# Optimization experiments

Measured on AMD Instinct MI355X. Metric: run time of the kernel, lower is better.

Reference implementation:

```python
import jax, jax.numpy as jnp
import numpy as np

N_VERBS = 500
N_ROLES = 190
VOCAB = 2000
R = 6            # max_role_count
EMB = 512        # embed_hidden == lstm_hidden
MLP = 1024       # mlp_hidden
C = 512          # conv base size
H = W = 7
NP = H * W
NC = C + 2       # conv channels + 2 coord channels


def _lin(k, fan_in, fan_out):
    kw, kb = jax.random.split(k)
    s = 1.0 / np.sqrt(fan_in)
    return (jax.random.uniform(kw, (fan_in, fan_out), jnp.float32, -s, s),
            jax.random.uniform(kb, (fan_out,), jnp.float32, -s, s))


def setup_inputs() -> dict:
    key = jax.random.key(0)
    ks = jax.random.split(key, 16)
    inp = {}
    inp['conv_feat'] = jax.random.normal(ks[0], (2, C, H, W), jnp.float32)
    inp['verbs'] = jax.random.randint(ks[1], (2,), 0, N_VERBS, jnp.int32)
    inp['roles'] = jax.random.randint(ks[2], (2, R), 0, N_ROLES, jnp.int32)
    inp['verb_emb'] = jax.random.normal(ks[3], (N_VERBS, EMB), jnp.float32)
    inp['role_emb'] = jax.random.normal(ks[4], (N_ROLES + 1, EMB), jnp.float32)
    inp['vW1'], inp['vb1'] = _lin(ks[5], NP * C, MLP)
    inp['vW2'], inp['vb2'] = _lin(ks[6], MLP, MLP)
    inp['vW3'], inp['vb3'] = _lin(ks[7], MLP, N_VERBS)
    inp['gW1'], inp['gb1'] = _lin(ks[8], 2 * NC + EMB, MLP)
    inp['gW2'], inp['gb2'] = _lin(ks[9], MLP, MLP)
    inp['gW3'], inp['gb3'] = _lin(ks[10], MLP, 2 * MLP)
    inp['gW4'], inp['gb4'] = _lin(ks[11], 2 * MLP, 4 * MLP)
    inp['fW1'], inp['fb1'] = _lin(ks[12], 4 * MLP, 4 * MLP)
    inp['fW2'], inp['fb2'] = _lin(ks[13], 4 * MLP, 2 * MLP)
    inp['fW3'], inp['fb3'] = _lin(ks[14], 2 * MLP, VOCAB)
    return inp


def _coords():
    c = jnp.linspace(-4.0, 4.0, H)
    x = jnp.broadcast_to(c[None, :], (H, W))   # x varies along width
    y = jnp.broadcast_to(c[:, None], (H, W))   # y varies along height
    return jnp.stack([x, y]).reshape(2, NP).T  # [NP, 2]


def reference(conv_feat, verbs, roles, verb_emb, role_emb,
              vW1, vb1, vW2, vb2, vW3, vb3,
              gW1, gb1, gW2, gb2, gW3, gb3, gW4, gb4,
              fW1, fb1, fW2, fb2, fW3, fb3):
    relu = jax.nn.relu
    B = conv_feat.shape[0]

    # verb head
    flat = conv_feat.reshape(B, NP * C)
    v = relu(flat @ vW1 + vb1)
    v = relu(v @ vW2 + vb2)
    verb_pred = v @ vW3 + vb3                                  # [B, N_VERBS]

    # role-verb query
    rv = (verb_emb[verbs][:, None, :] * role_emb[roles]).reshape(B * R, EMB)

    # per-role conv features + coord channels -> [Bu, NP, NC]
    feat = jnp.broadcast_to(conv_feat[:, None], (B, R, C, H, W)).reshape(B * R, C, NP)
    feat = jnp.concatenate([feat.transpose(0, 2, 1),
                            jnp.broadcast_to(_coords()[None], (B * R, NP, 2))], axis=2)

    # first g layer: concat([o_j, o_i, qst]) @ gW1 == split matmuls + broadcast add
    Wa, Wb, Wc = gW1[:NC], gW1[NC:2 * NC], gW1[2 * NC:]
    A = feat @ Wa          # pairs with conv1 (index j)
    Bm = feat @ Wb         # pairs with conv2 (index i)
    Q = rv @ Wc
    h = relu(A[:, None, :, :] + Bm[:, :, None, :] + Q[:, None, None, :] + gb1)  # [Bu, NP, NP, MLP]
    h = relu(h @ gW2 + gb2)
    h = relu(h @ gW3 + gb3)
    h = relu(h @ gW4 + gb4)                                    # [Bu, NP, NP, 4*MLP]
    g = h.sum(axis=(1, 2))                                     # [Bu, 4*MLP]

    f = relu(g @ fW1 + fb1)
    f = relu(f @ fW2 + fb2)
    f = f @ fW3 + fb3                                          # [Bu, VOCAB]
    role_predict = f.reshape(B, R, VOCAB)
    return verb_pred, role_predict
```

## Files before the change

kernel.cpp:

```cpp
#include <hip/hip_runtime.h>
#include <cstdint>

typedef _Float16 f16;
typedef f16 f16x8 __attribute__((ext_vector_type(8)));
typedef f16 f16x4 __attribute__((ext_vector_type(4)));
typedef float f32x4 __attribute__((ext_vector_type(4)));

#define GROUP_ROWS 2560
#define VALID_ROWS 2401
#define TPG 10
#define NGROUP 12

template <bool B> struct BoolC { static constexpr bool value = B; };

__device__ __forceinline__ void gll16(const void* g, void* l) {
  __builtin_amdgcn_global_load_lds((const __attribute__((address_space(1))) void*)g,
                                   (__attribute__((address_space(3))) void*)l, 16, 0, 0);
}

__global__ void wtrans_all(const float* __restrict__ gW2, const float* __restrict__ gW3,
                           const float* __restrict__ gW4, f16* __restrict__ W2t,
                           f16* __restrict__ W3t, f16* __restrict__ W4t) {
  __shared__ float t[32][33];
  int blk = blockIdx.x;
  const float* W; f16* Wt; int K, N, local;
  if (blk < 1024)      { W = gW2; Wt = W2t; K = 1024; N = 1024; local = blk; }
  else if (blk < 3072) { W = gW3; Wt = W3t; K = 1024; N = 2048; local = blk - 1024; }
  else                 { W = gW4; Wt = W4t; K = 2048; N = 4096; local = blk - 3072; }
  int ntn = N >> 5;
  int k0 = (local / ntn) * 32, n0 = (local % ntn) * 32;
  int tx = threadIdx.x & 31, ty = threadIdx.x >> 5;
#pragma unroll
  for (int j = 0; j < 4; ++j)
    t[ty + j * 8][tx] = W[(size_t)(k0 + ty + j * 8) * N + n0 + tx];
  __syncthreads();
#pragma unroll
  for (int j = 0; j < 4; ++j)
    Wt[(size_t)(n0 + ty + j * 8) * K + k0 + tx] = (f16)t[tx][ty + j * 8];
}

__global__ void build_rv(const float* __restrict__ verb_emb, const float* __restrict__ role_emb,
                         const int* __restrict__ verbs, const int* __restrict__ roles,
                         float* __restrict__ rv) {
  int g = blockIdx.x;
  int b = g / 6;
  int v = verbs[b], ro = roles[g];
  for (int e = threadIdx.x; e < 512; e += 256)
    rv[g * 512 + e] = verb_emb[(size_t)v * 512 + e] * role_emb[(size_t)ro * 512 + e];
}

__global__ void build_AB(const float* __restrict__ conv, const float* __restrict__ gW1,
                         float* __restrict__ A, float* __restrict__ Bm) {
  int blk = blockIdx.x;
  int nq = blk & 3, bp = blk >> 2;
  int p = bp % 49, b = bp / 49;
  int n = nq * 256 + threadIdx.x;
  float accA = 0.f, accB = 0.f;
  for (int k = 0; k < 514; ++k) {
    float s;
    if (k < 512) s = conv[((size_t)b * 512 + k) * 49 + p];
    else {
      int c7 = (k == 512) ? (p % 7) : (p / 7);
      s = (float)(c7 - 3) * (4.0f / 3.0f);
    }
    accA = fmaf(s, gW1[(size_t)k * 1024 + n], accA);
    accB = fmaf(s, gW1[(size_t)(514 + k) * 1024 + n], accB);
  }
  size_t row = ((size_t)b * 49 + p) * 1024;
  A[row + n] = accA;
  Bm[row + n] = accB;
}

__global__ void build_h1(const float* __restrict__ A, const float* __restrict__ Bm,
                         const float* __restrict__ Q, const float* __restrict__ gb1,
                         f16* __restrict__ h1, int g0) {
  int rc = blockIdx.x;
  int gl = rc / GROUP_ROWS;
  int li = rc % GROUP_ROWS;
  int g = g0 + gl;
  int b = g / 6;
  int kk = threadIdx.x * 4;
  f16x4* dst = (f16x4*)(h1 + (size_t)rc * 1024 + kk);
  if (li >= VALID_ROWS) {
    f16x4 z = {(f16)0.f, (f16)0.f, (f16)0.f, (f16)0.f};
    *dst = z;
    return;
  }
  int i = li / 49, j = li % 49;
  const float4 a = *(const float4*)(A + ((size_t)b * 49 + j) * 1024 + kk);
  const float4 bb = *(const float4*)(Bm + ((size_t)b * 49 + i) * 1024 + kk);
  const float4 q = *(const float4*)(Q + (size_t)g * 1024 + kk);
  const float4 bi = *(const float4*)(gb1 + kk);
  float v0 = a.x + bb.x + q.x + bi.x;
  float v1 = a.y + bb.y + q.y + bi.y;
  float v2 = a.z + bb.z + q.z + bi.z;
  float v3 = a.w + bb.w + q.w + bi.w;
  f16x4 r;
  r.x = (f16)(v0 > 0.f ? v0 : 0.f);
  r.y = (f16)(v1 > 0.f ? v1 : 0.f);
  r.z = (f16)(v2 > 0.f ? v2 : 0.f);
  r.w = (f16)(v3 > 0.f ? v3 : 0.f);
  *dst = r;
}

#define WV4 asm volatile("s_waitcnt vmcnt(4)" ::: "memory")
#define WV0 asm volatile("s_waitcnt vmcnt(0)" ::: "memory")

#define LDSA(buf, mf, cc) (*(const f16x8*)(ldsc + (buf)*32768 + arow + (mf)*2048 + (cc)*16))
#define LDSB(buf, nf, cc) (*(const f16x8*)(ldsc + 65536 + (buf)*32768 + brow + (nf)*2048 + (cc)*16))

#define LOADB(BF, buf) { \
  BF[0][0] = LDSB(buf, 0, c0); BF[0][1] = LDSB(buf, 0, c1); \
  BF[1][0] = LDSB(buf, 1, c0); BF[1][1] = LDSB(buf, 1, c1); \
  BF[2][0] = LDSB(buf, 2, c0); BF[2][1] = LDSB(buf, 2, c1); \
  BF[3][0] = LDSB(buf, 3, c0); BF[3][1] = LDSB(buf, 3, c1); }

#define STAGE_A(t, h) { \
  const f16* _g = Aglo + (long)(h) * (128L * K) + (long)(t) * 64; \
  char* _l = ldsc + ((t)&1)*32768 + ((h)*128 + wave*16)*128; \
  gll16(_g, _l); gll16(_g + 8L*K, _l + 1024); }

#define STAGE_B(t, h) { \
  const f16* _g = Bglo + (long)(h) * (128L * K) + (long)(t) * 64; \
  char* _l = ldsc + 65536 + ((t)&1)*32768 + ((h)*128 + wave*16)*128; \
  gll16(_g, _l); gll16(_g + 8L*K, _l + 1024); }

#define PHASE(q, buf, BF, STG, WT, POST) { \
  f16x8 a00 = LDSA(buf, 2*(q), c0);   f16x8 a01 = LDSA(buf, 2*(q), c1); \
  f16x8 a10 = LDSA(buf, 2*(q)+1, c0); f16x8 a11 = LDSA(buf, 2*(q)+1, c1); \
  STG; \
  WT; \
  __builtin_amdgcn_s_barrier(); \
  __builtin_amdgcn_s_setprio(1); \
  _Pragma("unroll") \
  for (int nf = 0; nf < 4; ++nf) { \
    acc[2*(q)][nf]   = __builtin_amdgcn_mfma_f32_16x16x32_f16(a00, BF[nf][0], acc[2*(q)][nf], 0, 0, 0); \
    acc[2*(q)][nf]   = __builtin_amdgcn_mfma_f32_16x16x32_f16(a01, BF[nf][1], acc[2*(q)][nf], 0, 0, 0); \
    acc[2*(q)+1][nf] = __builtin_amdgcn_mfma_f32_16x16x32_f16(a10, BF[nf][0], acc[2*(q)+1][nf], 0, 0, 0); \
    acc[2*(q)+1][nf] = __builtin_amdgcn_mfma_f32_16x16x32_f16(a11, BF[nf][1], acc[2*(q)+1][nf], 0, 0, 0); \
  } \
  __builtin_amdgcn_s_setprio(0); \
  POST; \
  __builtin_amdgcn_s_barrier(); \
}

template <int FUSED>
__global__ __launch_bounds__(512, 2)
void gemm256(const f16* __restrict__ A, const f16* __restrict__ Bt,
             const float* __restrict__ bias, f16* __restrict__ C,
             float* __restrict__ P, int N, int K, int ntiles, int mtile_off) {
  __shared__ __align__(16) char ldsbuf[131072];
  char* ldsc = ldsbuf;
  const int tid = threadIdx.x;
  const int wave = tid >> 6, lane = tid & 63;
  const int wm = wave >> 2, wn = wave & 3;
  const int lr = lane & 15, lk = lane >> 4;
  const int c0 = lk ^ (lr & 7), c1 = c0 ^ 4;
  const int arow = (wm * 128 + lr) * 128;
  const int brow = (wn * 64 + lr) * 128;

  int nwg = gridDim.x, id = blockIdx.x;
  int qq = nwg >> 3, rr8 = nwg & 7;
  int xcd = id & 7, idx = id >> 3;
  int wg = (xcd < rr8 ? xcd * (qq + 1) : rr8 * (qq + 1) + (xcd - rr8) * qq) + idx;
  const int mtile = wg / ntiles, ntile = wg % ntiles;
  const long m0 = (long)mtile * 256, n0 = (long)ntile * 256;

  const int srow = lane >> 3;
  const int schunk = (lane & 7) ^ srow;
  const f16* Aglo = A + (m0 + wave * 16 + srow) * (long)K + schunk * 8;
  const f16* Bglo = Bt + (n0 + wave * 16 + srow) * (long)K + schunk * 8;

  f32x4 acc[8][4] = {};
  f16x8 bFa[4][2], bFb[4][2];

  const int NI = K >> 7;

  STAGE_B(0, 0); STAGE_B(0, 1);
  STAGE_A(0, 0); STAGE_A(0, 1);
  STAGE_B(1, 0); STAGE_B(1, 1);
  WV4;
  __builtin_amdgcn_s_barrier();
  LOADB(bFa, 0);

  auto run_iter = [&](int i, auto lastTag) {
    constexpr bool LAST = decltype(lastTag)::value;
    PHASE(0, 0, bFa, STAGE_A(2*i+1, 0), ;, ;);
    PHASE(1, 0, bFa, STAGE_A(2*i+1, 1), ;, ;);
    PHASE(2, 0, bFa, if constexpr (!LAST) STAGE_B(2*i+2, 0), ;, ;);
    PHASE(3, 0, bFa, if constexpr (!LAST) STAGE_B(2*i+2, 1),
                 if constexpr (LAST) { WV0; } else { WV4; },
                 LOADB(bFb, 1));
    PHASE(0, 1, bFb, if constexpr (!LAST) STAGE_A(2*i+2, 0), ;, ;);
    PHASE(1, 1, bFb, if constexpr (!LAST) STAGE_A(2*i+2, 1), ;, ;);
    PHASE(2, 1, bFb, if constexpr (!LAST) STAGE_B(2*i+3, 0), ;, ;);
    PHASE(3, 1, bFb, if constexpr (!LAST) STAGE_B(2*i+3, 1),
                 if constexpr (!LAST) { WV4; },
                 if constexpr (!LAST) LOADB(bFa, 0));
  };
#pragma unroll 1
  for (int i = 0; i < NI - 1; ++i) run_iter(i, BoolC<false>{});
  run_iter(NI - 1, BoolC<true>{});

  if (FUSED == 0) {
#pragma unroll
    for (int mf = 0; mf < 8; ++mf) {
      const long row = m0 + wm * 128 + mf * 16 + lk * 4;
#pragma unroll
      for (int nf = 0; nf < 4; ++nf) {
        const long col = n0 + wn * 64 + nf * 16 + lr;
        const float bv = bias[col];
#pragma unroll
        for (int r = 0; r < 4; ++r) {
          float v = acc[mf][nf][r] + bv;
          v = v > 0.f ? v : 0.f;
          C[(row + r) * N + col] = (f16)v;
        }
      }
    }
  } else {
    float* csum = (float*)ldsc;
    const int mrel = (mtile % TPG) * 256 + wm * 128;
#pragma unroll
    for (int nf = 0; nf < 4; ++nf) {
      const int col = (int)n0 + wn * 64 + nf * 16 + lr;
      const float bv = bias[col];
      float s = 0.f;
#pragma unroll
      for (int mf = 0; mf < 8; ++mf) {
        const int rb = mrel + mf * 16 + lk * 4;
#pragma unroll
        for (int r = 0; r < 4; ++r) {
          float v = acc[mf][nf][r] + bv;
          v = v > 0.f ? v : 0.f;
          if (rb + r < VALID_ROWS) s += v;
        }
      }
      s += __shfl_xor(s, 16);
      s += __shfl_xor(s, 32);
      if (lk == 0) csum[wm * 256 + wn * 64 + nf * 16 + lr] = s;
    }
    __syncthreads();
    for (int t = tid; t < 256; t += 512)
      P[(long)(mtile_off + mtile) * N + n0 + t] = csum[t] + csum[256 + t];
  }
}

__global__ void reduce_g(const float* __restrict__ P, float* __restrict__ g) {
  int idx = blockIdx.x * 256 + threadIdx.x;
  if (idx >= NGROUP * 4096) return;
  int gi = idx >> 12, n = idx & 4095;
  float s = 0.f;
#pragma unroll
  for (int t = 0; t < TPG; ++t) s += P[(size_t)(gi * TPG + t) * 4096 + n];
  g[idx] = s;
}

template <int M>
__global__ void skinny_part(const float* __restrict__ X, const float* __restrict__ W,
                            float* __restrict__ P, int K, int N, int kchunk) {
  int n = blockIdx.x * 256 + threadIdx.x;
  int k0 = blockIdx.y * kchunk;
  int k1 = k0 + kchunk;
  if (k1 > K) k1 = K;
  if (n >= N) return;
  float acc[M];
#pragma unroll
  for (int m = 0; m < M; ++m) acc[m] = 0.f;
  for (int k = k0; k < k1; ++k) {
    float w = W[(size_t)k * N + n];
#pragma unroll
    for (int m = 0; m < M; ++m) acc[m] = fmaf(X[(size_t)m * K + k], w, acc[m]);
  }
#pragma unroll
  for (int m = 0; m < M; ++m) P[((size_t)blockIdx.y * M + m) * N + n] = acc[m];
}

template <int RELU>
__global__ void skinny_fin(const float* __restrict__ P, const float* __restrict__ bias,
                           float* __restrict__ dst, int M, int N, int KC) {
  int idx = blockIdx.x * 256 + threadIdx.x;
  if (idx >= M * N) return;
  int m = idx / N, n = idx - m * N;
  float s = bias ? bias[n] : 0.f;
  for (int kc = 0; kc < KC; ++kc) s += P[((size_t)kc * M + m) * N + n];
  if (RELU) s = s > 0.f ? s : 0.f;
  dst[idx] = s;
}

static inline void skinny(const float* X, const float* W, const float* bias, float* dst,
                          float* sp, int Mrows, int K, int N, int relu, hipStream_t stream) {
  int KC = K >> 4;
  if (KC > 64) KC = 64;
  if (KC < 1) KC = 1;
  int kchunk = (K + KC - 1) / KC;
  dim3 g1((N + 255) / 256, KC);
  if (Mrows == 2)
    skinny_part<2><<<g1, 256, 0, stream>>>(X, W, sp, K, N, kchunk);
  else
    skinny_part<12><<<g1, 256, 0, stream>>>(X, W, sp, K, N, kchunk);
  int blocks = (Mrows * N + 255) / 256;
  if (relu)
    skinny_fin<1><<<blocks, 256, 0, stream>>>(sp, bias, dst, Mrows, N, KC);
  else
    skinny_fin<0><<<blocks, 256, 0, stream>>>(sp, bias, dst, Mrows, N, KC);
}

extern "C" void kernel_launch(void* const* d_in, const int* in_sizes, int n_in,
                              void* d_out, int out_size, void* d_ws, size_t ws_size,
                              hipStream_t stream) {
  const float* conv = (const float*)d_in[0];
  const int* verbs = (const int*)d_in[1];
  const int* roles = (const int*)d_in[2];
  const float* verb_emb = (const float*)d_in[3];
  const float* role_emb = (const float*)d_in[4];
  const float* vW1 = (const float*)d_in[5];
  const float* vb1 = (const float*)d_in[6];
  const float* vW2 = (const float*)d_in[7];
  const float* vb2 = (const float*)d_in[8];
  const float* vW3 = (const float*)d_in[9];
  const float* vb3 = (const float*)d_in[10];
  const float* gW1 = (const float*)d_in[11];
  const float* gb1 = (const float*)d_in[12];
  const float* gW2 = (const float*)d_in[13];
  const float* gb2 = (const float*)d_in[14];
  const float* gW3 = (const float*)d_in[15];
  const float* gb3 = (const float*)d_in[16];
  const float* gW4 = (const float*)d_in[17];
  const float* gb4 = (const float*)d_in[18];
  const float* fW1 = (const float*)d_in[19];
  const float* fb1 = (const float*)d_in[20];
  const float* fW2 = (const float*)d_in[21];
  const float* fb2 = (const float*)d_in[22];
  const float* fW3 = (const float*)d_in[23];
  const float* fb3 = (const float*)d_in[24];
  float* out = (float*)d_out;

  char* w = (char*)d_ws;
  auto alloc = [&](size_t bytes) {
    char* p = w;
    w += (bytes + 255) & ~(size_t)255;
    return p;
  };
  f16* W2t = (f16*)alloc((size_t)1024 * 1024 * 2);
  f16* W3t = (f16*)alloc((size_t)2048 * 1024 * 2);
  f16* W4t = (f16*)alloc((size_t)4096 * 2048 * 2);
  float* P4 = (float*)alloc((size_t)NGROUP * TPG * 4096 * 4);
  float* Abuf = (float*)alloc((size_t)2 * 49 * 1024 * 4);
  float* Bbuf = (float*)alloc((size_t)2 * 49 * 1024 * 4);
  float* Qbuf = (float*)alloc((size_t)12 * 1024 * 4);
  float* rvb = (float*)alloc((size_t)12 * 512 * 4);
  float* gbuf = (float*)alloc((size_t)12 * 4096 * 4);
  float* sp = (float*)alloc((size_t)64 * 12 * 4096 * 4);
  float* f1b = (float*)alloc((size_t)12 * 4096 * 4);
  float* f2b = (float*)alloc((size_t)12 * 2048 * 4);
  float* v1b = (float*)alloc((size_t)2 * 1024 * 4);
  float* v2b = (float*)alloc((size_t)2 * 1024 * 4);

  size_t used = (size_t)(w - (char*)d_ws);
  size_t remain = ws_size > used ? ws_size - used : 0;
  static const int opts[6] = {12, 6, 4, 3, 2, 1};
  int gpc = 1;
  for (int i = 0; i < 6; ++i) {
    size_t need = (size_t)opts[i] * GROUP_ROWS * 4096 * 2 + 4096;
    if (need <= remain) { gpc = opts[i]; break; }
  }
  f16* h1 = (f16*)alloc((size_t)gpc * GROUP_ROWS * 1024 * 2);
  f16* h2 = (f16*)alloc((size_t)gpc * GROUP_ROWS * 1024 * 2);
  f16* h3 = (f16*)alloc((size_t)gpc * GROUP_ROWS * 2048 * 2);
  int nchunks = NGROUP / gpc;

  wtrans_all<<<1024 + 2048 + 8192, 256, 0, stream>>>(gW2, gW3, gW4, W2t, W3t, W4t);

  build_rv<<<12, 256, 0, stream>>>(verb_emb, role_emb, verbs, roles, rvb);
  build_AB<<<98 * 4, 256, 0, stream>>>(conv, gW1, Abuf, Bbuf);
  skinny(rvb, gW1 + (size_t)1028 * 1024, nullptr, Qbuf, sp, 12, 512, 1024, 0, stream);

  skinny(conv, vW1, vb1, v1b, sp, 2, 25088, 1024, 1, stream);
  skinny(v1b, vW2, vb2, v2b, sp, 2, 1024, 1024, 1, stream);
  skinny(v2b, vW3, vb3, out, sp, 2, 1024, 500, 0, stream);

  for (int c = 0; c < nchunks; ++c) {
    int g0 = c * gpc;
    int Mc = gpc * GROUP_ROWS;
    int mt = Mc / 256;
    build_h1<<<Mc, 256, 0, stream>>>(Abuf, Bbuf, Qbuf, gb1, h1, g0);
    gemm256<0><<<4 * mt, 512, 0, stream>>>(h1, W2t, gb2, h2, nullptr, 1024, 1024, 4, 0);
    gemm256<0><<<8 * mt, 512, 0, stream>>>(h2, W3t, gb3, h3, nullptr, 2048, 1024, 8, 0);
    gemm256<1><<<16 * mt, 512, 0, stream>>>(h3, W4t, gb4, nullptr, P4, 4096, 2048, 16, g0 * TPG);
  }
  reduce_g<<<(NGROUP * 4096 + 255) / 256, 256, 0, stream>>>(P4, gbuf);

  skinny(gbuf, fW1, fb1, f1b, sp, 12, 4096, 4096, 1, stream);
  skinny(f1b, fW2, fb2, f2b, sp, 12, 4096, 2048, 1, stream);
  skinny(f2b, fW3, fb3, out + 1000, sp, 12, 2048, 2000, 0, stream);

  (void)in_sizes; (void)n_in; (void)out_size; (void)ws_size;
}
```

Baseline: 1.162 ms.

## Split-K AB build, stage GEMM epilogue through LDS, retune skinny split

Splits the A/B first-layer projection over eight K chunks with a separate reduction kernel, so more blocks run in parallel. Stages the non-fused GEMM epilogue through a swizzled LDS tile so stores become coalesced 16-byte row writes. Retunes the skinny split-K count to target about 1024 blocks and unrolls its inner loop. These add extra partial-sum buffer traffic and kernel launches. The split-K scratch must also fit in the shared sp buffer.

```diff
diff --git a/kernel.cpp b/kernel.cpp
--- a/kernel.cpp
+++ b/kernel.cpp
@@ -49,14 +49,17 @@
     rv[g * 512 + e] = verb_emb[(size_t)v * 512 + e] * role_emb[(size_t)ro * 512 + e];
 }
 
-__global__ void build_AB(const float* __restrict__ conv, const float* __restrict__ gW1,
-                         float* __restrict__ A, float* __restrict__ Bm) {
+__global__ void build_AB_part(const float* __restrict__ conv, const float* __restrict__ gW1,
+                              float* __restrict__ part) {
   int blk = blockIdx.x;
   int nq = blk & 3, bp = blk >> 2;
   int p = bp % 49, b = bp / 49;
   int n = nq * 256 + threadIdx.x;
+  int ky = blockIdx.y;
+  int k0 = ky * 66, k1 = k0 + 66;
+  if (k1 > 514) k1 = 514;
   float accA = 0.f, accB = 0.f;
-  for (int k = 0; k < 514; ++k) {
+  for (int k = k0; k < k1; ++k) {
     float s;
     if (k < 512) s = conv[((size_t)b * 512 + k) * 49 + p];
     else {
@@ -66,9 +69,21 @@
     accA = fmaf(s, gW1[(size_t)k * 1024 + n], accA);
     accB = fmaf(s, gW1[(size_t)(514 + k) * 1024 + n], accB);
   }
-  size_t row = ((size_t)b * 49 + p) * 1024;
-  A[row + n] = accA;
-  Bm[row + n] = accB;
+  size_t base = ((size_t)ky * 98 + bp) * 2048;
+  part[base + n] = accA;
+  part[base + 1024 + n] = accB;
+}
+
+__global__ void build_AB_fin(const float* __restrict__ part, float* __restrict__ A,
+                             float* __restrict__ Bm) {
+  int idx = blockIdx.x * 256 + threadIdx.x;
+  if (idx >= 98 * 2048) return;
+  int bp = idx >> 11, rem = idx & 2047;
+  float s = 0.f;
+#pragma unroll
+  for (int ky = 0; ky < 8; ++ky) s += part[((size_t)ky * 98 + bp) * 2048 + rem];
+  if (rem < 1024) A[(size_t)bp * 1024 + rem] = s;
+  else Bm[(size_t)bp * 1024 + (rem - 1024)] = s;
 }
 
 __global__ void build_h1(const float* __restrict__ A, const float* __restrict__ Bm,
@@ -203,20 +218,31 @@
   run_iter(NI - 1, BoolC<true>{});
 
   if (FUSED == 0) {
+    __syncthreads();
+    f16* lt = (f16*)ldsc;
 #pragma unroll
     for (int mf = 0; mf < 8; ++mf) {
-      const long row = m0 + wm * 128 + mf * 16 + lk * 4;
 #pragma unroll
       for (int nf = 0; nf < 4; ++nf) {
-        const long col = n0 + wn * 64 + nf * 16 + lr;
-        const float bv = bias[col];
+        const int col = wn * 64 + nf * 16 + lr;
+        const float bv = bias[n0 + col];
 #pragma unroll
         for (int r = 0; r < 4; ++r) {
+          const int row = wm * 128 + mf * 16 + lk * 4 + r;
           float v = acc[mf][nf][r] + bv;
           v = v > 0.f ? v : 0.f;
-          C[(row + r) * N + col] = (f16)v;
+          lt[row * 256 + (col ^ (((row >> 2) & 3) << 4))] = (f16)v;
         }
       }
+    }
+    __syncthreads();
+    const int r0 = tid >> 5, ch = tid & 31;
+#pragma unroll
+    for (int p = 0; p < 16; ++p) {
+      const int row = p * 16 + r0;
+      const int chs = ch ^ (((row >> 2) & 3) << 1);
+      f16x8 v = *(const f16x8*)(lt + row * 256 + chs * 8);
+      *(f16x8*)(C + (m0 + row) * N + n0 + ch * 8) = v;
     }
   } else {
     float* csum = (float*)ldsc;
@@ -267,6 +293,7 @@
   float acc[M];
 #pragma unroll
   for (int m = 0; m < M; ++m) acc[m] = 0.f;
+#pragma unroll 4
   for (int k = k0; k < k1; ++k) {
     float w = W[(size_t)k * N + n];
 #pragma unroll
@@ -290,11 +317,14 @@
 
 static inline void skinny(const float* X, const float* W, const float* bias, float* dst,
                           float* sp, int Mrows, int K, int N, int relu, hipStream_t stream) {
-  int KC = K >> 4;
-  if (KC > 64) KC = 64;
-  if (KC < 1) KC = 1;
+  int nx = (N + 255) / 256;
+  int KC = 1024 / nx;
+  if (KC > 256) KC = 256;
+  int kmax = K / 16;
+  if (kmax < 1) kmax = 1;
+  if (KC > kmax) KC = kmax;
   int kchunk = (K + KC - 1) / KC;
-  dim3 g1((N + 255) / 256, KC);
+  dim3 g1(nx, KC);
   if (Mrows == 2)
     skinny_part<2><<<g1, 256, 0, stream>>>(X, W, sp, K, N, kchunk);
   else
@@ -373,7 +403,8 @@
   wtrans_all<<<1024 + 2048 + 8192, 256, 0, stream>>>(gW2, gW3, gW4, W2t, W3t, W4t);
 
   build_rv<<<12, 256, 0, stream>>>(verb_emb, role_emb, verbs, roles, rvb);
-  build_AB<<<98 * 4, 256, 0, stream>>>(conv, gW1, Abuf, Bbuf);
+  build_AB_part<<<dim3(98 * 4, 8), 256, 0, stream>>>(conv, gW1, sp);
+  build_AB_fin<<<(98 * 2048 + 255) / 256, 256, 0, stream>>>(sp, Abuf, Bbuf);
   skinny(rvb, gW1 + (size_t)1028 * 1024, nullptr, Qbuf, sp, 12, 512, 1024, 0, stream);
 
   skinny(conv, vW1, vb1, v1b, sp, 2, 25088, 1024, 1, stream);
```

Measured after the change: 934.5 us. 1.24x faster.
